# Optimization experiments

Measured on AMD Instinct MI355X. Metric: run time of the kernel, lower is better.

The kernel has to match this reference:

```python
import jax, jax.numpy as jnp
import numpy as np

DIM = 128
HEADS = 4


def setup_inputs() -> dict:
    key = jax.random.key(0)
    ks = jax.random.split(key, 6)
    B_, N, C = 2048, 49, DIM
    nW = 64
    x = jax.random.normal(ks[0], (B_, N, C), dtype=jnp.float32)
    mask = jax.random.normal(ks[1], (nW, N, N), dtype=jnp.float32)
    qkv_w = jax.random.normal(ks[2], (3 * C, C), dtype=jnp.float32) * 0.02
    qkv_b = jnp.zeros((3 * C,), dtype=jnp.float32)
    proj_w = jax.random.normal(ks[3], (C, C), dtype=jnp.float32) * 0.02
    proj_b = jnp.zeros((C,), dtype=jnp.float32)
    return {"x": x, "mask": mask, "qkv_w": qkv_w, "qkv_b": qkv_b,
            "proj_w": proj_w, "proj_b": proj_b}


def reference(x, mask, qkv_w, qkv_b, proj_w, proj_b):
    B_, N, C = x.shape
    H = HEADS
    Dh = C // H
    scale = Dh ** (-0.5)
    # fused QKV projection: [B_, N, 3C]
    qkv = x @ qkv_w.T + qkv_b
    qkv = qkv.reshape(B_, N, 3, H, Dh).transpose(2, 0, 3, 1, 4)  # [3, B_, H, N, Dh]
    q, k, v = qkv[0] * scale, qkv[1], qkv[2]
    attn = jnp.einsum('bhqd,bhkd->bhqk', q, k)  # [B_, H, N, N]
    nW = mask.shape[0]
    # add per-window additive mask: broadcast over images and heads
    attn = attn.reshape(B_ // nW, nW, H, N, N) + mask[None, :, None, :, :]
    attn = jax.nn.softmax(attn.reshape(B_, H, N, N), axis=-1)
    out = jnp.einsum('bhqk,bhkd->bhqd', attn, v)  # [B_, H, N, Dh]
    out = out.transpose(0, 2, 1, 3).reshape(B_, N, C)
    return out @ proj_w.T + proj_b
```

## Files before the change

### kernel.cpp

```cpp
#include <hip/hip_runtime.h>

typedef __bf16 bf16_t;
typedef __bf16 bf16x2 __attribute__((ext_vector_type(2)));
typedef __bf16 bf16x4 __attribute__((ext_vector_type(4)));
typedef __bf16 bf16x8 __attribute__((ext_vector_type(8)));
typedef float  f32x4  __attribute__((ext_vector_type(4)));
typedef float  f32x4u __attribute__((ext_vector_type(4), aligned(4)));
typedef unsigned int u32;

#define MFMA16(a, b, c) __builtin_amdgcn_mfma_f32_16x16x32_bf16((a), (b), (c), 0, 0, 0)

#define SMEM_BYTES 76800


union W8 { u32 u[4]; bf16x8 v; };

__device__ __forceinline__ u32 pack2(float a, float b) {
    union { bf16x2 h; u32 u; } c;
    c.h[0] = (bf16_t)a; c.h[1] = (bf16_t)b;
    return c.u;
}

__global__ void wconv_kernel(const float* __restrict__ qw, const float* __restrict__ pw,
                             bf16_t* __restrict__ o) {
    int i = (blockIdx.x * 256 + threadIdx.x) * 4;
    const float* src = (i < 49152) ? (qw + i) : (pw + (i - 49152));
    float4 f = *(const float4*)src;
    bf16x4 h;
    h[0] = (bf16_t)f.x; h[1] = (bf16_t)f.y; h[2] = (bf16_t)f.z; h[3] = (bf16_t)f.w;
    *(bf16x4*)(o + i) = h;
}

__device__ __forceinline__ bf16x8 ldw(const float* __restrict__ wf,
                                      const bf16_t* __restrict__ wb,
                                      int use_b, int idx) {
    if (use_b) {
        return *(const bf16x8*)(wb + idx);
    } else {
        float4 f0 = *(const float4*)(wf + idx);
        float4 f1 = *(const float4*)(wf + idx + 4);
        bf16x8 r;
        r[0] = (bf16_t)f0.x; r[1] = (bf16_t)f0.y; r[2] = (bf16_t)f0.z; r[3] = (bf16_t)f0.w;
        r[4] = (bf16_t)f1.x; r[5] = (bf16_t)f1.y; r[6] = (bf16_t)f1.z; r[7] = (bf16_t)f1.w;
        return r;
    }
}

__global__ __launch_bounds__(512, 4) void winattn_kernel(
    const float* __restrict__ xg, const float* __restrict__ maskg,
    const float* __restrict__ qwg, const float* __restrict__ qbg,
    const float* __restrict__ pwg, const float* __restrict__ pbg,
    const bf16_t* __restrict__ wqb, const bf16_t* __restrict__ wpb,
    const int use_wbf, const int nW, float* __restrict__ outg)
{
    extern __shared__ char smem[];
    bf16_t* xatt = (bf16_t*)smem;

    const int b    = blockIdx.x;
    const int tid  = threadIdx.x;
    const int w    = tid >> 6;
    const int lane = tid & 63;
    const int g    = lane >> 4;
    const int c0   = lane & 15;

    {
        const float4* xb = (const float4*)(xg + (long)b * 6272);
        #pragma unroll 4
        for (int i = tid; i < 1568; i += 512) {
            float4 f = xb[i];
            int row = i >> 5;
            int col = (i & 31) << 2;
            bf16x4 hq;
            hq[0] = (bf16_t)f.x; hq[1] = (bf16_t)f.y; hq[2] = (bf16_t)f.z; hq[3] = (bf16_t)f.w;
            *(bf16x4*)(xatt + row * 136 + col) = hq;
        }
        unsigned int* z = (unsigned int*)(xatt + 49 * 136);
        for (int i = tid; i < 1020; i += 512) z[i] = 0u;
    }
    __syncthreads();

    {
        const int oqk = 32 * w;
        float4 biasqk[2];
        #pragma unroll
        for (int nt = 0; nt < 2; ++nt)
            biasqk[nt] = *(const float4*)(qbg + oqk + 16 * nt + 4 * g);
        float biasv = qbg[256 + 16 * w + c0];
        const float scale = 0.17677669529663687f;
        const float qmul  = (w < 4) ? scale : 1.0f;

        f32x4 aqk[2][4], av[4];
        #pragma unroll
        for (int nt = 0; nt < 2; ++nt)
            #pragma unroll
            for (int mt = 0; mt < 4; ++mt) aqk[nt][mt] = {0.f, 0.f, 0.f, 0.f};
        #pragma unroll
        for (int mt = 0; mt < 4; ++mt) av[mt] = {0.f, 0.f, 0.f, 0.f};

        #pragma unroll
        for (int ks = 0; ks < 4; ++ks) {
            bf16x8 wqk[2], wv;
            #pragma unroll
            for (int nt = 0; nt < 2; ++nt)
                wqk[nt] = ldw(qwg, wqb, use_wbf, (oqk + 16 * nt + c0) * 128 + 32 * ks + 8 * g);
            wv = ldw(qwg, wqb, use_wbf, (256 + 16 * w + c0) * 128 + 32 * ks + 8 * g);
            bf16x8 xf[4];
            #pragma unroll
            for (int mt = 0; mt < 4; ++mt)
                xf[mt] = *(const bf16x8*)(xatt + (16 * mt + c0) * 136 + 32 * ks + 8 * g);
            #pragma unroll
            for (int nt = 0; nt < 2; ++nt)
                #pragma unroll
                for (int mt = 0; mt < 4; ++mt)
                    aqk[nt][mt] = MFMA16(wqk[nt], xf[mt], aqk[nt][mt]);
            #pragma unroll
            for (int mt = 0; mt < 4; ++mt)
                av[mt] = MFMA16(xf[mt], wv, av[mt]);
        }

        #pragma unroll
        for (int nt = 0; nt < 2; ++nt) {
            int oh  = (oqk + 16 * nt) & 127;
            int hh  = oh >> 5;
            int dh0 = 16 * nt  + 4 * g;
            bf16_t* base = (bf16_t*)(smem + 17408 + hh * 14848) + (w < 4 ? 0 : 2560);
            #pragma unroll
            for (int mt = 0; mt < 4; ++mt) {
                int tok = 16 * mt + c0;
                bf16x4 t;
                t[0] = (bf16_t)((aqk[nt][mt][0] + biasqk[nt].x) * qmul);
                t[1] = (bf16_t)((aqk[nt][mt][1] + biasqk[nt].y) * qmul);
                t[2] = (bf16_t)((aqk[nt][mt][2] + biasqk[nt].z) * qmul);
                t[3] = (bf16_t)((aqk[nt][mt][3] + biasqk[nt].w) * qmul);
                *(bf16x4*)(base + tok * 40 + dh0) = t;
            }
        }
        {
            int dhv = 16 * (w & 1) + c0;
            bf16_t* vt = (bf16_t*)(smem + 17408 + (w >> 1) * 14848) + 5120;
            #pragma unroll
            for (int mt = 0; mt < 4; ++mt) {
                bf16x4 t;
                t[0] = (bf16_t)(av[mt][0] + biasv);
                t[1] = (bf16_t)(av[mt][1] + biasv);
                t[2] = (bf16_t)(av[mt][2] + biasv);
                t[3] = (bf16_t)(av[mt][3] + biasv);
                *(bf16x4*)(vt + dhv * 72 + 16 * mt + 4 * g) = t;
            }
        }
    }
    __syncthreads();

    const int h   = w >> 1;
    const int qh2 = w & 1;
    bf16_t* qls = (bf16_t*)(smem + 17408 + h * 14848);
    bf16_t* kls = qls + 2560;
    bf16_t* vls = qls + 5120;

    bf16x8 pwf[4];
    #pragma unroll
    for (int ks = 0; ks < 4; ++ks)
        pwf[ks] = ldw(pwg, wpb, use_wbf, (16 * w + c0) * 128 + 32 * ks + 8 * g);
    float4 pbias4 = *(const float4*)(pbg + 16 * w + 4 * g);

    float mv[2][16];
    {
        const float* mrow = maskg + (long)(b % nW) * 2401;
        #pragma unroll
        for (int nt = 0; nt < 2; ++nt) {
            int q  = (qh2 * 2 + nt) * 16 + c0;
            int qm = q < 49 ? q : 48;
            const float* mr = mrow + qm * 49;
            f32x4u m0 = *(const f32x4u*)(mr + 4 * g);
            f32x4u m1 = *(const f32x4u*)(mr + 16 + 4 * g);
            f32x4u m2 = *(const f32x4u*)(mr + 32 + 4 * g);
            float m48 = mr[48];
            #pragma unroll
            for (int r = 0; r < 4; ++r) {
                mv[nt][0 + r] = m0[r];
                mv[nt][4 + r] = m1[r];
                mv[nt][8 + r] = m2[r];
            }
            mv[nt][12] = (g == 0) ? m48 : -1e30f;
            mv[nt][13] = -1e30f; mv[nt][14] = -1e30f; mv[nt][15] = -1e30f;
        }
    }

    bf16x8 ka[4], qb2[2];
    #pragma unroll
    for (int mt = 0; mt < 4; ++mt)
        ka[mt] = *(const bf16x8*)(kls + (16 * mt + c0) * 40 + 8 * g);
    #pragma unroll
    for (int nt = 0; nt < 2; ++nt)
        qb2[nt] = *(const bf16x8*)(qls + ((qh2 * 2 + nt) * 16 + c0) * 40 + 8 * g);

    bf16x8 pa[2][2];
    const bool gl = (g & 1) != 0, gh = (g & 2) != 0;
    #pragma unroll
    for (int nt = 0; nt < 2; ++nt) {
        f32x4 s[4];
        #pragma unroll
        for (int mt = 0; mt < 4; ++mt) s[mt] = {0.f, 0.f, 0.f, 0.f};
        #pragma unroll
        for (int mt = 0; mt < 4; ++mt)
            s[mt] = MFMA16(ka[mt], qb2[nt], s[mt]);

        float lg[16];
        float m = -1e30f;
        #pragma unroll
        for (int mt = 0; mt < 4; ++mt)
            #pragma unroll
            for (int r = 0; r < 4; ++r) {
                float v = s[mt][r] + mv[nt][mt * 4 + r];
                lg[mt * 4 + r] = v;
                m = fmaxf(m, v);
            }
        m = fmaxf(m, __shfl_xor(m, 16));
        m = fmaxf(m, __shfl_xor(m, 32));
        float sum = 0.f;
        #pragma unroll
        for (int i = 0; i < 16; ++i) { float e = __expf(lg[i] - m); lg[i] = e; sum += e; }
        sum += __shfl_xor(sum, 16);
        sum += __shfl_xor(sum, 32);
        float inv = 1.f / sum;

        u32 wd[8];
        #pragma unroll
        for (int j = 0; j < 8; ++j) {
            int mt = j >> 1, rb = (j & 1) * 2;
            wd[j] = pack2(lg[mt * 4 + rb] * inv, lg[mt * 4 + rb + 1] * inv);
        }
        u32 X[8], Y[8], Z[8];
        #pragma unroll
        for (int j = 0; j < 8; ++j) X[j] = __shfl_xor(wd[j], 16);
        #pragma unroll
        for (int j = 0; j < 8; ++j) Y[j] = __shfl_xor(wd[j], 32);
        #pragma unroll
        for (int j = 0; j < 8; ++j) Z[j] = __shfl_xor(X[j], 32);
        #pragma unroll
        for (int ks = 0; ks < 2; ++ks) {
            W8 u;
            #pragma unroll
            for (int t = 0; t < 4; ++t) {
                int j0 = 4 * ks + (t & 1);
                int j1 = j0 + 2;
                u32 lo, hi;
                if (t < 2) { lo = gl ? Z[j0] : wd[j0]; hi = gl ? X[j1] : Y[j1]; }
                else       { lo = gl ? Y[j0] : X[j0];  hi = gl ? wd[j1] : Z[j1]; }
                u.u[t] = gh ? hi : lo;
            }
            pa[nt][ks] = u.v;
        }
    }

    {
        f32x4 o2[2][2];
        #pragma unroll
        for (int nt = 0; nt < 2; ++nt)
            #pragma unroll
            for (int dt = 0; dt < 2; ++dt) o2[nt][dt] = {0.f, 0.f, 0.f, 0.f};
        #pragma unroll
        for (int ks = 0; ks < 2; ++ks) {
            bf16x8 vf[2];
            #pragma unroll
            for (int dt = 0; dt < 2; ++dt)
                vf[dt] = *(const bf16x8*)(vls + (16 * dt + c0) * 72 + 32 * ks + 8 * g);
            #pragma unroll
            for (int nt = 0; nt < 2; ++nt)
                #pragma unroll
                for (int dt = 0; dt < 2; ++dt)
                    o2[nt][dt] = MFMA16(pa[nt][ks], vf[dt], o2[nt][dt]);
        }
        #pragma unroll
        for (int nt = 0; nt < 2; ++nt)
            #pragma unroll
            for (int dt = 0; dt < 2; ++dt)
                #pragma unroll
                for (int r = 0; r < 4; ++r) {
                    int q = (qh2 * 2 + nt) * 16 + 4 * g + r;
                    xatt[q * 136 + 32 * h + 16 * dt + c0] = (bf16_t)o2[nt][dt][r];
                }
    }
    __syncthreads();

    {
        f32x4 acc[4];
        #pragma unroll
        for (int mt = 0; mt < 4; ++mt) acc[mt] = {0.f, 0.f, 0.f, 0.f};
        #pragma unroll
        for (int ks = 0; ks < 4; ++ks) {
            bf16x8 af[4];
            #pragma unroll
            for (int mt = 0; mt < 4; ++mt)
                af[mt] = *(const bf16x8*)(xatt + (16 * mt + c0) * 136 + 32 * ks + 8 * g);
            #pragma unroll
            for (int mt = 0; mt < 4; ++mt)
                acc[mt] = MFMA16(pwf[ks], af[mt], acc[mt]);
        }
        float* ob = outg + (long)b * 6272;
        #pragma unroll
        for (int mt = 0; mt < 4; ++mt) {
            int tok = 16 * mt + c0;
            if (tok < 49) {
                float4 t;
                t.x = acc[mt][0] + pbias4.x;
                t.y = acc[mt][1] + pbias4.y;
                t.z = acc[mt][2] + pbias4.z;
                t.w = acc[mt][3] + pbias4.w;
                *(float4*)(ob + tok * 128 + 16 * w + 4 * g) = t;
            }
        }
    }
}

extern "C" void kernel_launch(void* const* d_in, const int* in_sizes, int n_in,
                              void* d_out, int out_size, void* d_ws, size_t ws_size,
                              hipStream_t stream) {
    const float* xg  = (const float*)d_in[0];
    const float* mg  = (const float*)d_in[1];
    const float* qwg = (const float*)d_in[2];
    const float* qbg = (const float*)d_in[3];
    const float* pwg = (const float*)d_in[4];
    const float* pbg = (const float*)d_in[5];
    float* outg = (float*)d_out;

    const int B  = in_sizes[0] / (49 * 128);
    const int nW = in_sizes[1] / (49 * 49);

    int use_wbf = (d_ws != nullptr && ws_size >= 131072) ? 1 : 0;
    bf16_t* wqb = (bf16_t*)d_ws;
    bf16_t* wpb = use_wbf ? (wqb + 49152) : nullptr;
    if (use_wbf)
        wconv_kernel<<<64, 256, 0, stream>>>(qwg, pwg, wqb);

    (void)hipFuncSetAttribute((const void*)winattn_kernel,
                              hipFuncAttributeMaxDynamicSharedMemorySize, SMEM_BYTES);

    winattn_kernel<<<B, 512, SMEM_BYTES, stream>>>(
        xg, mg, qwg, qbg, pwg, pbg, wqb, use_wbf ? wpb : wqb, use_wbf, nW, outg);
}
```

Measured before the change: 64.55 us.

## Keep Q in registers and alias K/V over x buffer to halve LDS

The QKV projection is reorganised so each wave computes its own head's Q tile and keeps it in registers, redistributing it into MFMA operand layout with lane shuffles instead of staging Q in LDS. K and V are written into regions that alias the x staging buffer, with extra barriers, which cuts dynamic shared memory from about 75KB to 38KB and raises the launch-bounds occupancy target from 4 to 6. The attention stage now processes one query tile at a time, and the P·V product is computed transposed. This should allow more resident blocks per CU to hide latency, at the cost of duplicated Q projection work across the two waves per head, extra synchronisation, and more register pressure.

```diff
diff --git a/kernel.cpp b/kernel.cpp
--- a/kernel.cpp
+++ b/kernel.cpp
@@ -10,7 +10,7 @@
 
 #define MFMA16(a, b, c) __builtin_amdgcn_mfma_f32_16x16x32_bf16((a), (b), (c), 0, 0, 0)
 
-#define SMEM_BYTES 76800
+#define SMEM_BYTES 38912
 
 
 union W8 { u32 u[4]; bf16x8 v; };
@@ -19,6 +19,30 @@
     union { bf16x2 h; u32 u; } c;
     c.h[0] = (bf16_t)a; c.h[1] = (bf16_t)b;
     return c.u;
+}
+
+__device__ __forceinline__ void redist(const u32 wd[8], bf16x8 out[2], bool gl, bool gh) {
+    u32 X[8], Y[8], Z[8];
+    #pragma unroll
+    for (int j = 0; j < 8; ++j) X[j] = __shfl_xor(wd[j], 16);
+    #pragma unroll
+    for (int j = 0; j < 8; ++j) Y[j] = __shfl_xor(wd[j], 32);
+    #pragma unroll
+    for (int j = 0; j < 8; ++j) Z[j] = __shfl_xor(X[j], 32);
+    #pragma unroll
+    for (int fi = 0; fi < 2; ++fi) {
+        W8 u;
+        #pragma unroll
+        for (int t = 0; t < 4; ++t) {
+            int j0 = 4 * fi + (t & 1);
+            int j1 = j0 + 2;
+            u32 lo, hi;
+            if (t < 2) { lo = gl ? Z[j0] : wd[j0]; hi = gl ? X[j1] : Y[j1]; }
+            else       { lo = gl ? Y[j0] : X[j0];  hi = gl ? wd[j1] : Z[j1]; }
+            u.u[t] = gh ? hi : lo;
+        }
+        out[fi] = u.v;
+    }
 }
 
 __global__ void wconv_kernel(const float* __restrict__ qw, const float* __restrict__ pw,
@@ -46,7 +70,7 @@
     }
 }
 
-__global__ __launch_bounds__(512, 4) void winattn_kernel(
+__global__ __launch_bounds__(512, 6) void winattn_kernel(
     const float* __restrict__ xg, const float* __restrict__ maskg,
     const float* __restrict__ qwg, const float* __restrict__ qbg,
     const float* __restrict__ pwg, const float* __restrict__ pbg,
@@ -55,6 +79,8 @@
 {
     extern __shared__ char smem[];
     bf16_t* xatt = (bf16_t*)smem;
+    bf16_t* kreg = (bf16_t*)smem;
+    bf16_t* vreg = (bf16_t*)(smem + 20480);
 
     const int b    = blockIdx.x;
     const int tid  = threadIdx.x;
@@ -62,113 +88,159 @@
     const int lane = tid & 63;
     const int g    = lane >> 4;
     const int c0   = lane & 15;
+    const int h    = w >> 1;
+    const int qh2  = w & 1;
+    const bool gl  = (g & 1) != 0, gh = (g & 2) != 0;
+
+    const int qrow  = 32 * h;
+    const int kvrow = 128 + 32 * w;
 
     {
         const float4* xb = (const float4*)(xg + (long)b * 6272);
-        #pragma unroll 4
-        for (int i = tid; i < 1568; i += 512) {
+        #pragma unroll
+        for (int it = 0; it < 3; ++it) {
+            int i = tid + it * 512;
             float4 f = xb[i];
-            int row = i >> 5;
-            int col = (i & 31) << 2;
+            int row = i >> 5, col = (i & 31) << 2;
             bf16x4 hq;
             hq[0] = (bf16_t)f.x; hq[1] = (bf16_t)f.y; hq[2] = (bf16_t)f.z; hq[3] = (bf16_t)f.w;
             *(bf16x4*)(xatt + row * 136 + col) = hq;
         }
+        if (tid < 32) {
+            int i = tid + 1536;
+            float4 f = xb[i];
+            int row = i >> 5, col = (i & 31) << 2;
+            bf16x4 hq;
+            hq[0] = (bf16_t)f.x; hq[1] = (bf16_t)f.y; hq[2] = (bf16_t)f.z; hq[3] = (bf16_t)f.w;
+            *(bf16x4*)(xatt + row * 136 + col) = hq;
+        }
         unsigned int* z = (unsigned int*)(xatt + 49 * 136);
         for (int i = tid; i < 1020; i += 512) z[i] = 0u;
     }
     __syncthreads();
 
+    f32x4 qacc[2][2];
+    f32x4 kv0[4], kv1[4];
+    #pragma unroll
+    for (int i = 0; i < 2; ++i)
+        #pragma unroll
+        for (int j = 0; j < 2; ++j) qacc[i][j] = {0.f, 0.f, 0.f, 0.f};
+    #pragma unroll
+    for (int mt = 0; mt < 4; ++mt) { kv0[mt] = {0.f, 0.f, 0.f, 0.f}; kv1[mt] = {0.f, 0.f, 0.f, 0.f}; }
+
+    #pragma unroll
+    for (int ks = 0; ks < 4; ++ks) {
+        bf16x8 wq0 = ldw(qwg, wqb, use_wbf, (qrow + c0) * 128 + 32 * ks + 8 * g);
+        bf16x8 wq1 = ldw(qwg, wqb, use_wbf, (qrow + 16 + c0) * 128 + 32 * ks + 8 * g);
+        bf16x8 wkv = ldw(qwg, wqb, use_wbf, (kvrow + c0) * 128 + 32 * ks + 8 * g);
+        bf16x8 xf[4];
+        #pragma unroll
+        for (int mt = 0; mt < 4; ++mt)
+            xf[mt] = *(const bf16x8*)(xatt + (16 * mt + c0) * 136 + 32 * ks + 8 * g);
+        #pragma unroll
+        for (int ntq = 0; ntq < 2; ++ntq) {
+            qacc[ntq][0] = MFMA16(wq0, xf[2 * qh2 + ntq], qacc[ntq][0]);
+            qacc[ntq][1] = MFMA16(wq1, xf[2 * qh2 + ntq], qacc[ntq][1]);
+        }
+        if (w < 4) {
+            #pragma unroll
+            for (int mt = 0; mt < 4; ++mt) kv0[mt] = MFMA16(wkv, xf[mt], kv0[mt]);
+        } else {
+            #pragma unroll
+            for (int mt = 0; mt < 4; ++mt) kv0[mt] = MFMA16(xf[mt], wkv, kv0[mt]);
+        }
+    }
+
+    if (w >= 4) {
+        float bv = qbg[kvrow + c0];
+        bf16_t* vt = vreg + (w - 4) * 2304;
+        #pragma unroll
+        for (int mt = 0; mt < 4; ++mt) {
+            bf16x4 t;
+            t[0] = (bf16_t)(kv0[mt][0] + bv); t[1] = (bf16_t)(kv0[mt][1] + bv);
+            t[2] = (bf16_t)(kv0[mt][2] + bv); t[3] = (bf16_t)(kv0[mt][3] + bv);
+            *(bf16x4*)(vt + c0 * 72 + 16 * mt + 4 * g) = t;
+        }
+    }
+
+    bf16x8 qb2[2];
     {
-        const int oqk = 32 * w;
-        float4 biasqk[2];
-        #pragma unroll
-        for (int nt = 0; nt < 2; ++nt)
-            biasqk[nt] = *(const float4*)(qbg + oqk + 16 * nt + 4 * g);
-        float biasv = qbg[256 + 16 * w + c0];
-        const float scale = 0.17677669529663687f;
-        const float qmul  = (w < 4) ? scale : 1.0f;
-
-        f32x4 aqk[2][4], av[4];
-        #pragma unroll
-        for (int nt = 0; nt < 2; ++nt)
-            #pragma unroll
-            for (int mt = 0; mt < 4; ++mt) aqk[nt][mt] = {0.f, 0.f, 0.f, 0.f};
-        #pragma unroll
-        for (int mt = 0; mt < 4; ++mt) av[mt] = {0.f, 0.f, 0.f, 0.f};
-
-        #pragma unroll
-        for (int ks = 0; ks < 4; ++ks) {
-            bf16x8 wqk[2], wv;
-            #pragma unroll
-            for (int nt = 0; nt < 2; ++nt)
-                wqk[nt] = ldw(qwg, wqb, use_wbf, (oqk + 16 * nt + c0) * 128 + 32 * ks + 8 * g);
-            wv = ldw(qwg, wqb, use_wbf, (256 + 16 * w + c0) * 128 + 32 * ks + 8 * g);
-            bf16x8 xf[4];
-            #pragma unroll
-            for (int mt = 0; mt < 4; ++mt)
-                xf[mt] = *(const bf16x8*)(xatt + (16 * mt + c0) * 136 + 32 * ks + 8 * g);
-            #pragma unroll
-            for (int nt = 0; nt < 2; ++nt)
-                #pragma unroll
-                for (int mt = 0; mt < 4; ++mt)
-                    aqk[nt][mt] = MFMA16(wqk[nt], xf[mt], aqk[nt][mt]);
-            #pragma unroll
-            for (int mt = 0; mt < 4; ++mt)
-                av[mt] = MFMA16(xf[mt], wv, av[mt]);
-        }
-
-        #pragma unroll
-        for (int nt = 0; nt < 2; ++nt) {
-            int oh  = (oqk + 16 * nt) & 127;
-            int hh  = oh >> 5;
-            int dh0 = 16 * nt  + 4 * g;
-            bf16_t* base = (bf16_t*)(smem + 17408 + hh * 14848) + (w < 4 ? 0 : 2560);
-            #pragma unroll
-            for (int mt = 0; mt < 4; ++mt) {
-                int tok = 16 * mt + c0;
-                bf16x4 t;
-                t[0] = (bf16_t)((aqk[nt][mt][0] + biasqk[nt].x) * qmul);
-                t[1] = (bf16_t)((aqk[nt][mt][1] + biasqk[nt].y) * qmul);
-                t[2] = (bf16_t)((aqk[nt][mt][2] + biasqk[nt].z) * qmul);
-                t[3] = (bf16_t)((aqk[nt][mt][3] + biasqk[nt].w) * qmul);
-                *(bf16x4*)(base + tok * 40 + dh0) = t;
-            }
-        }
+        const float qs = 0.17677669529663687f;
+        float4 qb40 = *(const float4*)(qbg + qrow + 4 * g);
+        float4 qb41 = *(const float4*)(qbg + qrow + 16 + 4 * g);
+        u32 wd[8];
+        #pragma unroll
+        for (int j = 0; j < 8; ++j) {
+            int ntq = j >> 2, mtq = (j >> 1) & 1, p = j & 1;
+            float b0 = mtq ? qb41[2 * p] : qb40[2 * p];
+            float b1 = mtq ? qb41[2 * p + 1] : qb40[2 * p + 1];
+            wd[j] = pack2((qacc[ntq][mtq][2 * p] + b0) * qs,
+                          (qacc[ntq][mtq][2 * p + 1] + b1) * qs);
+        }
+        redist(wd, qb2, gl, gh);
+    }
+
+    #pragma unroll
+    for (int ks = 0; ks < 4; ++ks) {
+        bf16x8 wkv = ldw(qwg, wqb, use_wbf, (kvrow + 16 + c0) * 128 + 32 * ks + 8 * g);
+        bf16x8 xf[4];
+        #pragma unroll
+        for (int mt = 0; mt < 4; ++mt)
+            xf[mt] = *(const bf16x8*)(xatt + (16 * mt + c0) * 136 + 32 * ks + 8 * g);
+        if (w < 4) {
+            #pragma unroll
+            for (int mt = 0; mt < 4; ++mt) kv1[mt] = MFMA16(wkv, xf[mt], kv1[mt]);
+        } else {
+            #pragma unroll
+            for (int mt = 0; mt < 4; ++mt) kv1[mt] = MFMA16(xf[mt], wkv, kv1[mt]);
+        }
+    }
+    if (w >= 4) {
+        float bv = qbg[kvrow + 16 + c0];
+        bf16_t* vt = vreg + (w - 4) * 2304;
+        #pragma unroll
+        for (int mt = 0; mt < 4; ++mt) {
+            bf16x4 t;
+            t[0] = (bf16_t)(kv1[mt][0] + bv); t[1] = (bf16_t)(kv1[mt][1] + bv);
+            t[2] = (bf16_t)(kv1[mt][2] + bv); t[3] = (bf16_t)(kv1[mt][3] + bv);
+            *(bf16x4*)(vt + (16 + c0) * 72 + 16 * mt + 4 * g) = t;
+        }
+    }
+    __syncthreads();
+
+    if (w < 4) {
+        float4 kb40 = *(const float4*)(qbg + kvrow + 4 * g);
+        float4 kb41 = *(const float4*)(qbg + kvrow + 16 + 4 * g);
+        bf16_t* kb = kreg + w * 2560;
+        #pragma unroll
+        for (int mt = 0; mt < 4; ++mt) {
+            int tok = 16 * mt + c0;
+            bf16x4 t0, t1;
+            t0[0] = (bf16_t)(kv0[mt][0] + kb40.x); t0[1] = (bf16_t)(kv0[mt][1] + kb40.y);
+            t0[2] = (bf16_t)(kv0[mt][2] + kb40.z); t0[3] = (bf16_t)(kv0[mt][3] + kb40.w);
+            t1[0] = (bf16_t)(kv1[mt][0] + kb41.x); t1[1] = (bf16_t)(kv1[mt][1] + kb41.y);
+            t1[2] = (bf16_t)(kv1[mt][2] + kb41.z); t1[3] = (bf16_t)(kv1[mt][3] + kb41.w);
+            *(bf16x4*)(kb + tok * 40 + 4 * g)      = t0;
+            *(bf16x4*)(kb + tok * 40 + 16 + 4 * g) = t1;
+        }
+    }
+    __syncthreads();
+
+    bf16_t* khead = kreg + h * 2560;
+    bf16x8 ka[4];
+    #pragma unroll
+    for (int mt = 0; mt < 4; ++mt)
+        ka[mt] = *(const bf16x8*)(khead + (16 * mt + c0) * 40 + 8 * g);
+    __syncthreads();
+
+    const float* mrow = maskg + (long)(b % nW) * 2401;
+    bf16_t* vhead = vreg + h * 2304;
+
+    #pragma unroll
+    for (int nt = 0; nt < 2; ++nt) {
+        float mv[16];
         {
-            int dhv = 16 * (w & 1) + c0;
-            bf16_t* vt = (bf16_t*)(smem + 17408 + (w >> 1) * 14848) + 5120;
-            #pragma unroll
-            for (int mt = 0; mt < 4; ++mt) {
-                bf16x4 t;
-                t[0] = (bf16_t)(av[mt][0] + biasv);
-                t[1] = (bf16_t)(av[mt][1] + biasv);
-                t[2] = (bf16_t)(av[mt][2] + biasv);
-                t[3] = (bf16_t)(av[mt][3] + biasv);
-                *(bf16x4*)(vt + dhv * 72 + 16 * mt + 4 * g) = t;
-            }
-        }
-    }
-    __syncthreads();
-
-    const int h   = w >> 1;
-    const int qh2 = w & 1;
-    bf16_t* qls = (bf16_t*)(smem + 17408 + h * 14848);
-    bf16_t* kls = qls + 2560;
-    bf16_t* vls = qls + 5120;
-
-    bf16x8 pwf[4];
-    #pragma unroll
-    for (int ks = 0; ks < 4; ++ks)
-        pwf[ks] = ldw(pwg, wpb, use_wbf, (16 * w + c0) * 128 + 32 * ks + 8 * g);
-    float4 pbias4 = *(const float4*)(pbg + 16 * w + 4 * g);
-
-    float mv[2][16];
-    {
-        const float* mrow = maskg + (long)(b % nW) * 2401;
-        #pragma unroll
-        for (int nt = 0; nt < 2; ++nt) {
-            int q  = (qh2 * 2 + nt) * 16 + c0;
+            int q  = 32 * qh2 + 16 * nt + c0;
             int qm = q < 49 ? q : 48;
             const float* mr = mrow + qm * 49;
             f32x4u m0 = *(const f32x4u*)(mr + 4 * g);
@@ -176,28 +248,11 @@
             f32x4u m2 = *(const f32x4u*)(mr + 32 + 4 * g);
             float m48 = mr[48];
             #pragma unroll
-            for (int r = 0; r < 4; ++r) {
-                mv[nt][0 + r] = m0[r];
-                mv[nt][4 + r] = m1[r];
-                mv[nt][8 + r] = m2[r];
-            }
-            mv[nt][12] = (g == 0) ? m48 : -1e30f;
-            mv[nt][13] = -1e30f; mv[nt][14] = -1e30f; mv[nt][15] = -1e30f;
-        }
-    }
-
-    bf16x8 ka[4], qb2[2];
-    #pragma unroll
-    for (int mt = 0; mt < 4; ++mt)
-        ka[mt] = *(const bf16x8*)(kls + (16 * mt + c0) * 40 + 8 * g);
-    #pragma unroll
-    for (int nt = 0; nt < 2; ++nt)
-        qb2[nt] = *(const bf16x8*)(qls + ((qh2 * 2 + nt) * 16 + c0) * 40 + 8 * g);
-
-    bf16x8 pa[2][2];
-    const bool gl = (g & 1) != 0, gh = (g & 2) != 0;
-    #pragma unroll
-    for (int nt = 0; nt < 2; ++nt) {
+            for (int r = 0; r < 4; ++r) { mv[r] = m0[r]; mv[4 + r] = m1[r]; mv[8 + r] = m2[r]; }
+            mv[12] = (g == 0) ? m48 : -1e30f;
+            mv[13] = -1e30f; mv[14] = -1e30f; mv[15] = -1e30f;
+        }
+
         f32x4 s[4];
         #pragma unroll
         for (int mt = 0; mt < 4; ++mt) s[mt] = {0.f, 0.f, 0.f, 0.f};
@@ -211,7 +266,7 @@
         for (int mt = 0; mt < 4; ++mt)
             #pragma unroll
             for (int r = 0; r < 4; ++r) {
-                float v = s[mt][r] + mv[nt][mt * 4 + r];
+                float v = s[mt][r] + mv[mt * 4 + r];
                 lg[mt * 4 + r] = v;
                 m = fmaxf(m, v);
             }
@@ -230,57 +285,33 @@
             int mt = j >> 1, rb = (j & 1) * 2;
             wd[j] = pack2(lg[mt * 4 + rb] * inv, lg[mt * 4 + rb + 1] * inv);
         }
-        u32 X[8], Y[8], Z[8];
-        #pragma unroll
-        for (int j = 0; j < 8; ++j) X[j] = __shfl_xor(wd[j], 16);
-        #pragma unroll
-        for (int j = 0; j < 8; ++j) Y[j] = __shfl_xor(wd[j], 32);
-        #pragma unroll
-        for (int j = 0; j < 8; ++j) Z[j] = __shfl_xor(X[j], 32);
+        bf16x8 pa[2];
+        redist(wd, pa, gl, gh);
+
+        f32x4 oo[2];
+        oo[0] = {0.f, 0.f, 0.f, 0.f}; oo[1] = {0.f, 0.f, 0.f, 0.f};
         #pragma unroll
         for (int ks = 0; ks < 2; ++ks) {
-            W8 u;
-            #pragma unroll
-            for (int t = 0; t < 4; ++t) {
-                int j0 = 4 * ks + (t & 1);
-                int j1 = j0 + 2;
-                u32 lo, hi;
-                if (t < 2) { lo = gl ? Z[j0] : wd[j0]; hi = gl ? X[j1] : Y[j1]; }
-                else       { lo = gl ? Y[j0] : X[j0];  hi = gl ? wd[j1] : Z[j1]; }
-                u.u[t] = gh ? hi : lo;
-            }
-            pa[nt][ks] = u.v;
-        }
-    }
-
-    {
-        f32x4 o2[2][2];
-        #pragma unroll
-        for (int nt = 0; nt < 2; ++nt)
-            #pragma unroll
-            for (int dt = 0; dt < 2; ++dt) o2[nt][dt] = {0.f, 0.f, 0.f, 0.f};
-        #pragma unroll
-        for (int ks = 0; ks < 2; ++ks) {
-            bf16x8 vf[2];
-            #pragma unroll
-            for (int dt = 0; dt < 2; ++dt)
-                vf[dt] = *(const bf16x8*)(vls + (16 * dt + c0) * 72 + 32 * ks + 8 * g);
-            #pragma unroll
-            for (int nt = 0; nt < 2; ++nt)
-                #pragma unroll
-                for (int dt = 0; dt < 2; ++dt)
-                    o2[nt][dt] = MFMA16(pa[nt][ks], vf[dt], o2[nt][dt]);
-        }
-        #pragma unroll
-        for (int nt = 0; nt < 2; ++nt)
-            #pragma unroll
-            for (int dt = 0; dt < 2; ++dt)
-                #pragma unroll
-                for (int r = 0; r < 4; ++r) {
-                    int q = (qh2 * 2 + nt) * 16 + 4 * g + r;
-                    xatt[q * 136 + 32 * h + 16 * dt + c0] = (bf16_t)o2[nt][dt][r];
-                }
-    }
+            bf16x8 va0 = *(const bf16x8*)(vhead + c0 * 72 + 32 * ks + 8 * g);
+            bf16x8 va1 = *(const bf16x8*)(vhead + (16 + c0) * 72 + 32 * ks + 8 * g);
+            oo[0] = MFMA16(va0, pa[ks], oo[0]);
+            oo[1] = MFMA16(va1, pa[ks], oo[1]);
+        }
+        int tok = 32 * qh2 + 16 * nt + c0;
+        #pragma unroll
+        for (int dt = 0; dt < 2; ++dt) {
+            bf16x4 t;
+            t[0] = (bf16_t)oo[dt][0]; t[1] = (bf16_t)oo[dt][1];
+            t[2] = (bf16_t)oo[dt][2]; t[3] = (bf16_t)oo[dt][3];
+            *(bf16x4*)(xatt + tok * 136 + 32 * h + 16 * dt + 4 * g) = t;
+        }
+    }
+
+    bf16x8 pwf[4];
+    #pragma unroll
+    for (int ks = 0; ks < 4; ++ks)
+        pwf[ks] = ldw(pwg, wpb, use_wbf, (16 * w + c0) * 128 + 32 * ks + 8 * g);
+    float4 pbias4 = *(const float4*)(pbg + 16 * w + 4 * g);
     __syncthreads();
 
     {
@@ -333,9 +364,6 @@
     if (use_wbf)
         wconv_kernel<<<64, 256, 0, stream>>>(qwg, pwg, wqb);
 
-    (void)hipFuncSetAttribute((const void*)winattn_kernel,
-                              hipFuncAttributeMaxDynamicSharedMemorySize, SMEM_BYTES);
-
     winattn_kernel<<<B, 512, SMEM_BYTES, stream>>>(
         xg, mg, qwg, qbg, pwg, pbg, wqb, use_wbf ? wpb : wqb, use_wbf, nW, outg);
 }
```

Result: slower. 116.8 us (+81.0%).
